# Performance work log

Measured on AMD Instinct MI355X. Metric: run time of the kernel, lower is better.

## Reference

```python
import jax, jax.numpy as jnp
import numpy as np

EPS = 1e-05
BITW = 8
BITA = 8


def _ste_round(v):
    # round with identity gradient (TF Round->Identity override)
    return v + jax.lax.stop_gradient(jnp.round(v) - v)


def _quantize_overflow(x, bits):
    # tensorlayer _quantize_overflow: linear quantization over [min, max]
    n = 2.0 ** bits - 1.0
    mx = jnp.max(x)
    mn = jnp.min(x)
    step = jax.lax.stop_gradient((mx - mn) / n)
    return _ste_round((x - mn) / step) * step + mn


def _conv2d_same(x, w):
    # x: [N,H,W,C], w: [KH,KW,C,F]
    return jax.lax.conv_general_dilated(
        x, w, window_strides=(1, 1), padding='SAME',
        dimension_numbers=('NHWC', 'HWIO', 'NHWC'))


def setup_inputs() -> dict:
    key = jax.random.key(0)
    k1, k2 = jax.random.split(key)
    x = jax.random.normal(k1, (32, 56, 56, 128), dtype=jnp.float32)
    W = jax.random.normal(k2, (3, 3, 128, 256), dtype=jnp.float32) * 0.02
    gamma = jnp.ones((256,), dtype=jnp.float32)
    beta = jnp.zeros((256,), dtype=jnp.float32)
    return {"x": x, "W": W, "gamma": gamma, "beta": beta}


def reference(x, W, gamma, beta):
    # 1) fake-quantize activations
    xq = _quantize_overflow(x, BITA)
    # 2) full-precision conv to get batch statistics (training path)
    conv_out = _conv2d_same(x, W)  # [N,H,W,F]
    mean = jnp.mean(conv_out, axis=(0, 1, 2))          # [F]
    var = jnp.var(conv_out, axis=(0, 1, 2))            # [F], biased (tf.nn.moments)
    inv_std = 1.0 / jnp.sqrt(var + EPS)                # [F]
    # 3) fold BN into weights/bias
    w_fold = W * (gamma * inv_std)                     # broadcast over [KH,KW,C,F]
    bias_fold = beta - gamma * mean * inv_std          # [F]
    # 4) quantize folded weights, conv with quantized activations
    wq = _quantize_overflow(w_fold, BITW)
    out = _conv2d_same(xq, wq) + bias_fold
    return jax.nn.relu(out)
```

## Files before the change

### kernel.cpp

```cpp
#include <hip/hip_runtime.h>

typedef float f32x4_t __attribute__((ext_vector_type(4)));
typedef __bf16 bf16x8_t __attribute__((ext_vector_type(8)));
typedef unsigned short u16x8_t __attribute__((ext_vector_type(8)));

#define NPIX        100352
#define PIX_PER_IMG 3136
#define PH          58
#define PPIX        3364
#define C_IN        128
#define C_OUT       256
#define NTAPS       9
#define NV4         3211264
#define NWELEM      294912
#define MTILES      392
#define NPADPIX     107648

#define OFF_ENC     0
#define OFF_SCALE   64
#define OFF_BIAS    1152
#define OFF_WT      4096
#define OFF_WQT     593920
#define OFF_PSUM    1183744
#define OFF_PSQ     1986560
#define OFF_XPAD    2789376
#define OFF_XQPAD   30347264

__device__ __forceinline__ unsigned short f2bf(float x) {
  unsigned u = __float_as_uint(x);
  u += 0x7FFFu + ((u >> 16) & 1u);
  return (unsigned short)(u >> 16);
}
__device__ __forceinline__ unsigned encf(float v) {
  unsigned u = __float_as_uint(v);
  return (u & 0x80000000u) ? ~u : (u | 0x80000000u);
}
__device__ __forceinline__ float decf(unsigned e) {
  unsigned u = (e & 0x80000000u) ? (e ^ 0x80000000u) : ~e;
  return __uint_as_float(u);
}
__device__ __forceinline__ void gl_lds16(const void* g, void* l) {
  auto gp = (const __attribute__((address_space(1))) unsigned*)(const unsigned*)g;
  auto lp = (__attribute__((address_space(3))) unsigned*)(unsigned*)l;
  __builtin_amdgcn_global_load_lds(gp, lp, 16, 0, 0);
}
#define SCHED_FENCE() __builtin_amdgcn_sched_barrier(0)

__global__ void kinit(unsigned* enc) {
  enc[0] = 0xFFFFFFFFu;
  enc[1] = 0u;
  enc[2] = 0xFFFFFFFFu;
  enc[3] = 0u;
}

__global__ void kminmax(const float4* __restrict__ x, unsigned* __restrict__ enc) {
  const int tid = blockIdx.x * blockDim.x + threadIdx.x;
  const int stride = gridDim.x * blockDim.x;
  float mn = 3.4e38f, mx = -3.4e38f;
  for (int i = tid; i < NV4; i += stride) {
    float4 v = x[i];
    mn = fminf(mn, fminf(fminf(v.x, v.y), fminf(v.z, v.w)));
    mx = fmaxf(mx, fmaxf(fmaxf(v.x, v.y), fmaxf(v.z, v.w)));
  }
  #pragma unroll
  for (int off = 32; off > 0; off >>= 1) {
    mn = fminf(mn, __shfl_xor(mn, off));
    mx = fmaxf(mx, __shfl_xor(mx, off));
  }
  __shared__ float smn[4], smx[4];
  const int lane = threadIdx.x & 63, w = threadIdx.x >> 6;
  if (lane == 0) { smn[w] = mn; smx[w] = mx; }
  __syncthreads();
  if (threadIdx.x == 0) {
    mn = fminf(fminf(smn[0], smn[1]), fminf(smn[2], smn[3]));
    mx = fmaxf(fmaxf(smx[0], smx[1]), fmaxf(smx[2], smx[3]));
    atomicMin(&enc[0], encf(mn));
    atomicMax(&enc[1], encf(mx));
  }
}

__global__ void kwconv(const float* __restrict__ W, unsigned short* __restrict__ wt) {
  const int idx = blockIdx.x * 256 + threadIdx.x;
  if (idx >= NWELEM) return;
  const int c = idx & 127;
  const int f = (idx >> 7) & 255;
  const int tap = idx >> 15;
  wt[idx] = f2bf(W[(tap * 128 + c) * 256 + f]);
}

__global__ void kwq(const float* __restrict__ W, const float* __restrict__ scale,
                    const unsigned* __restrict__ enc, unsigned short* __restrict__ wqt) {
  const int idx = blockIdx.x * 256 + threadIdx.x;
  if (idx >= NWELEM) return;
  const int c = idx & 127;
  const int f = (idx >> 7) & 255;
  const int tap = idx >> 15;
  const float wmn = decf(enc[2]), wmx = decf(enc[3]);
  const float wstep = (wmx - wmn) / 255.0f;
  const float wrstep = 255.0f / (wmx - wmn);
  const float v = W[(tap * 128 + c) * 256 + f] * scale[f];
  const float q = rintf((v - wmn) * wrstep) * wstep + wmn;
  wqt[idx] = f2bf(q);
}

__global__ void kpadfill(const float* __restrict__ x, const unsigned* __restrict__ enc,
                         unsigned short* __restrict__ xpad, unsigned short* __restrict__ xqpad)
{
  const int tid = blockIdx.x * 256 + threadIdx.x;
  if (tid >= NPADPIX * 16) return;
  const int pp = tid >> 4;
  const int c8 = (tid & 15) << 3;
  const int n = pp / PPIX;
  const int rem = pp - n * PPIX;
  const int hp = rem / PH;
  const int wp = rem - hp * PH;
  u16x8_t vb, vq;
  #pragma unroll
  for (int j = 0; j < 8; ++j) { vb[j] = 0; vq[j] = 0; }
  if (hp >= 1 && hp <= 56 && wp >= 1 && wp <= 56) {
    const float mn = decf(enc[0]), mx = decf(enc[1]);
    const float step = (mx - mn) / 255.0f, rstep = 255.0f / (mx - mn);
    const float* src = x + ((n * PIX_PER_IMG) + (hp - 1) * 56 + (wp - 1)) * C_IN + c8;
    const float4 a = *(const float4*)src;
    const float4 b = *(const float4*)(src + 4);
    const float v[8] = {a.x, a.y, a.z, a.w, b.x, b.y, b.z, b.w};
    #pragma unroll
    for (int j = 0; j < 8; ++j) {
      vb[j] = f2bf(v[j]);
      const float qv = rintf((v[j] - mn) * rstep) * step + mn;
      vq[j] = f2bf(qv);
    }
  }
  *(u16x8_t*)(xpad + pp * C_IN + c8) = vb;
  *(u16x8_t*)(xqpad + pp * C_IN + c8) = vq;
}

template<int STATS>
__global__ __launch_bounds__(512, 2)
void kconv(const unsigned short* __restrict__ xin,
           const unsigned short* __restrict__ wt,
           float* __restrict__ out,
           const float* __restrict__ bias,
           float* __restrict__ psum,
           float* __restrict__ psq)
{
  const int bid = blockIdx.x;
  const int bm = (bid & 7) * 49 + (bid >> 3);

  const int tid = threadIdx.x;
  const int lane = tid & 63;
  const int wid = tid >> 6;
  const int wm = wid >> 2;
  const int wn = wid & 3;
  const int l16 = lane & 15;
  const int rsub = lane >> 4;

  __shared__ __align__(16) unsigned char smem[131072];

  const int lchunk = (tid & 7) ^ ((tid >> 3) & 7);

  unsigned aoff[4];
  #pragma unroll
  for (int j = 0; j < 4; ++j) {
    const int pix = bm * 256 + j * 64 + (tid >> 3);
    const int n = pix / PIX_PER_IMG;
    const int rem = pix - n * PIX_PER_IMG;
    const int hh = rem / 56;
    const int ww = rem - hh * 56;
    aoff[j] = (unsigned)((n * PPIX + hh * PH + ww) * C_IN + lchunk * 8);
  }
  unsigned boff[4];
  #pragma unroll
  for (int j = 0; j < 4; ++j) {
    const int f = j * 64 + (tid >> 3);
    boff[j] = (unsigned)(f * C_IN + lchunk * 8);
  }

  f32x4_t acc[8][4];
  #pragma unroll
  for (int im = 0; im < 8; ++im)
    #pragma unroll
    for (int in = 0; in < 4; ++in)
      #pragma unroll
      for (int j = 0; j < 4; ++j) acc[im][in][j] = 0.f;

  auto stage = [&](int bsel, int s) {
    const int tap = s >> 1;
    const int chalf = (s & 1) << 6;
    const int kh = tap / 3, kw = tap - kh * 3;
    const unsigned atap = (unsigned)((kh * PH + kw) * C_IN + chalf);
    const unsigned btap = (unsigned)(tap * C_OUT * C_IN + chalf);
    unsigned char* sA = smem + bsel * 65536;
    unsigned char* sB = sA + 32768;
    #pragma unroll
    for (int j = 0; j < 4; ++j)
      gl_lds16(xin + atap + aoff[j], sA + j * 8192 + wid * 1024);
    #pragma unroll
    for (int j = 0; j < 4; ++j)
      gl_lds16(wt + btap + boff[j], sB + j * 8192 + wid * 1024);
  };

  auto compute = [&](int bsel) {
    const unsigned char* sA = smem + bsel * 65536;
    const unsigned char* sB = sA + 32768;
    #pragma unroll
    for (int ks = 0; ks < 2; ++ks) {
      const int c = ks * 4 + rsub;
      const int p = c ^ (l16 & 7);
      bf16x8_t av[8], bv[4];
      #pragma unroll
      for (int im = 0; im < 8; ++im)
        av[im] = *(const bf16x8_t*)(sA + (wm * 128 + im * 16 + l16) * 128 + p * 16);
      #pragma unroll
      for (int in = 0; in < 4; ++in)
        bv[in] = *(const bf16x8_t*)(sB + (wn * 64 + in * 16 + l16) * 128 + p * 16);
      #pragma unroll
      for (int im = 0; im < 8; ++im)
        #pragma unroll
        for (int in = 0; in < 4; ++in)
          acc[im][in] = __builtin_amdgcn_mfma_f32_16x16x32_bf16(av[im], bv[in], acc[im][in], 0, 0, 0);
    }
  };

  stage(0, 0);
  stage(1, 1);

  #pragma unroll 1
  for (int t = 0; t < 17; ++t) {
    asm volatile("s_waitcnt vmcnt(8)" ::: "memory");
    SCHED_FENCE();
    __builtin_amdgcn_s_barrier();
    SCHED_FENCE();
    compute(t & 1);
    SCHED_FENCE();
    __builtin_amdgcn_s_barrier();
    SCHED_FENCE();
    if (t < 16) stage(t & 1, t + 2);
  }
  asm volatile("s_waitcnt vmcnt(0)" ::: "memory");
  SCHED_FENCE();
  __builtin_amdgcn_s_barrier();
  SCHED_FENCE();
  compute(1);

  if (STATS) {
    float* sb = (float*)smem;
    #pragma unroll
    for (int in = 0; in < 4; ++in) {
      float s = 0.f, q = 0.f;
      #pragma unroll
      for (int im = 0; im < 8; ++im)
        #pragma unroll
        for (int j = 0; j < 4; ++j) {
          const float v = acc[im][in][j];
          s += v; q += v * v;
        }
      s += __shfl_xor(s, 16); q += __shfl_xor(q, 16);
      s += __shfl_xor(s, 32); q += __shfl_xor(q, 32);
      if (lane < 16) {
        sb[wid * 64 + in * 16 + lane] = s;
        sb[512 + wid * 64 + in * 16 + lane] = q;
      }
    }
    __syncthreads();
    if (tid < 256) {
      const int wn2 = tid >> 6, cl = tid & 63;
      const float s = sb[wn2 * 64 + cl] + sb[(4 + wn2) * 64 + cl];
      const float q = sb[512 + wn2 * 64 + cl] + sb[512 + (4 + wn2) * 64 + cl];
      psum[bm * 256 + tid] = s;
      psq[bm * 256 + tid] = q;
    }
  } else {
    float bval[4];
    #pragma unroll
    for (int in = 0; in < 4; ++in)
      bval[in] = bias[wn * 64 + in * 16 + l16];
    #pragma unroll
    for (int im = 0; im < 8; ++im) {
      #pragma unroll
      for (int j = 0; j < 4; ++j) {
        const int pix = bm * 256 + wm * 128 + im * 16 + rsub * 4 + j;
        #pragma unroll
        for (int in = 0; in < 4; ++in) {
          const int f = wn * 64 + in * 16 + l16;
          out[pix * 256 + f] = fmaxf(acc[im][in][j] + bval[in], 0.f);
        }
      }
    }
  }
}

__global__ __launch_bounds__(256)
void kstats(const float* __restrict__ psum, const float* __restrict__ psq,
            const float* __restrict__ gamma, const float* __restrict__ beta,
            float* __restrict__ scale, float* __restrict__ bias)
{
  const int ch = blockIdx.x;
  float s = 0.f, q = 0.f;
  for (int bm = threadIdx.x; bm < MTILES; bm += 256) {
    s += psum[bm * 256 + ch];
    q += psq[bm * 256 + ch];
  }
  #pragma unroll
  for (int off = 32; off > 0; off >>= 1) {
    s += __shfl_xor(s, off);
    q += __shfl_xor(q, off);
  }
  __shared__ float ss[4], sq2[4];
  const int lane = threadIdx.x & 63, w = threadIdx.x >> 6;
  if (lane == 0) { ss[w] = s; sq2[w] = q; }
  __syncthreads();
  if (threadIdx.x == 0) {
    s = ss[0] + ss[1] + ss[2] + ss[3];
    q = sq2[0] + sq2[1] + sq2[2] + sq2[3];
    const float inv = 1.0f / (float)NPIX;
    const float mean = s * inv;
    const float var = q * inv - mean * mean;
    const float istd = 1.0f / sqrtf(var + 1e-5f);
    const float g = gamma[ch];
    scale[ch] = g * istd;
    bias[ch] = beta[ch] - g * mean * istd;
  }
}

__global__ __launch_bounds__(256)
void kwmm(const float* __restrict__ W, const float* __restrict__ scale,
          unsigned* __restrict__ enc)
{
  const int idx = blockIdx.x * 256 + threadIdx.x;
  float v = 0.f;
  if (idx < NWELEM) v = W[idx] * scale[idx & 255];
  float mn = v, mx = v;
  #pragma unroll
  for (int off = 32; off > 0; off >>= 1) {
    mn = fminf(mn, __shfl_xor(mn, off));
    mx = fmaxf(mx, __shfl_xor(mx, off));
  }
  __shared__ float rmn[4], rmx[4];
  const int lane = threadIdx.x & 63, w = threadIdx.x >> 6;
  if (lane == 0) { rmn[w] = mn; rmx[w] = mx; }
  __syncthreads();
  if (threadIdx.x == 0) {
    mn = fminf(fminf(rmn[0], rmn[1]), fminf(rmn[2], rmn[3]));
    mx = fmaxf(fmaxf(rmx[0], rmx[1]), fmaxf(rmx[2], rmx[3]));
    atomicMin(&enc[2], encf(mn));
    atomicMax(&enc[3], encf(mx));
  }
}

extern "C" void kernel_launch(void* const* d_in, const int* in_sizes, int n_in,
                              void* d_out, int out_size, void* d_ws, size_t ws_size,
                              hipStream_t stream)
{
  const float* x     = (const float*)d_in[0];
  const float* W     = (const float*)d_in[1];
  const float* gamma = (const float*)d_in[2];
  const float* beta  = (const float*)d_in[3];
  float* out = (float*)d_out;
  char* ws = (char*)d_ws;

  unsigned* enc        = (unsigned*)(ws + OFF_ENC);
  float* scale         = (float*)(ws + OFF_SCALE);
  float* bias          = (float*)(ws + OFF_BIAS);
  unsigned short* Wt   = (unsigned short*)(ws + OFF_WT);
  unsigned short* Wqt  = (unsigned short*)(ws + OFF_WQT);
  float* psum          = (float*)(ws + OFF_PSUM);
  float* psq           = (float*)(ws + OFF_PSQ);
  unsigned short* xpad  = (unsigned short*)(ws + OFF_XPAD);
  unsigned short* xqpad = (unsigned short*)(ws + OFF_XQPAD);

  kinit<<<1, 64, 0, stream>>>(enc);
  kminmax<<<1024, 256, 0, stream>>>((const float4*)x, enc);
  kwconv<<<1152, 256, 0, stream>>>(W, Wt);
  kpadfill<<<6728, 256, 0, stream>>>(x, enc, xpad, xqpad);
  kconv<1><<<MTILES, 512, 0, stream>>>(xpad, Wt, nullptr, nullptr, psum, psq);
  kstats<<<256, 256, 0, stream>>>(psum, psq, gamma, beta, scale, bias);
  kwmm<<<1152, 256, 0, stream>>>(W, scale, enc);
  kwq<<<1152, 256, 0, stream>>>(W, scale, enc, Wqt);
  kconv<0><<<MTILES, 512, 0, stream>>>(xqpad, Wqt, out, bias, nullptr, nullptr);
}
```

Measured before the change: 230.4 us.

## Split conv tiles across output-channel halves and stream weights directly to registers

New measurement: 281.6 us. +22.2%, slower.

```diff
diff --git a/kernel.cpp b/kernel.cpp
--- a/kernel.cpp
+++ b/kernel.cpp
@@ -136,7 +136,7 @@
 }
 
 template<int STATS>
-__global__ __launch_bounds__(512, 2)
+__global__ __launch_bounds__(256, 2)
 void kconv(const unsigned short* __restrict__ xin,
            const unsigned short* __restrict__ wt,
            float* __restrict__ out,
@@ -145,36 +145,37 @@
            float* __restrict__ psq)
 {
   const int bid = blockIdx.x;
-  const int bm = (bid & 7) * 49 + (bid >> 3);
+  const int slot = (bid & 7) * 98 + (bid >> 3);
+  const int bm = slot >> 1;
+  const int bn = slot & 1;
 
   const int tid = threadIdx.x;
   const int lane = tid & 63;
   const int wid = tid >> 6;
-  const int wm = wid >> 2;
-  const int wn = wid & 3;
+  const int wm = wid >> 1;
+  const int wn = wid & 1;
   const int l16 = lane & 15;
   const int rsub = lane >> 4;
 
-  __shared__ __align__(16) unsigned char smem[131072];
-
-  const int lchunk = (tid & 7) ^ ((tid >> 3) & 7);
-
-  unsigned aoff[4];
-  #pragma unroll
-  for (int j = 0; j < 4; ++j) {
-    const int pix = bm * 256 + j * 64 + (tid >> 3);
+  __shared__ __align__(16) unsigned char smem[65536];
+
+  const int lchunk = (lane & 7) ^ ((lane >> 3) & 7);
+  unsigned aoff[8];
+  #pragma unroll
+  for (int j = 0; j < 8; ++j) {
+    const int pix = bm * 256 + j * 32 + wid * 8 + (lane >> 3);
     const int n = pix / PIX_PER_IMG;
     const int rem = pix - n * PIX_PER_IMG;
     const int hh = rem / 56;
     const int ww = rem - hh * 56;
     aoff[j] = (unsigned)((n * PPIX + hh * PH + ww) * C_IN + lchunk * 8);
   }
-  unsigned boff[4];
-  #pragma unroll
-  for (int j = 0; j < 4; ++j) {
-    const int f = j * 64 + (tid >> 3);
-    boff[j] = (unsigned)(f * C_IN + lchunk * 8);
-  }
+  unsigned boff[4][2];
+  #pragma unroll
+  for (int in = 0; in < 4; ++in)
+    #pragma unroll
+    for (int ks = 0; ks < 2; ++ks)
+      boff[in][ks] = (unsigned)((bn * 128 + wn * 64 + in * 16 + l16) * C_IN + (ks * 4 + rsub) * 8);
 
   f32x4_t acc[8][4];
   #pragma unroll
@@ -189,59 +190,65 @@
     const int chalf = (s & 1) << 6;
     const int kh = tap / 3, kw = tap - kh * 3;
     const unsigned atap = (unsigned)((kh * PH + kw) * C_IN + chalf);
-    const unsigned btap = (unsigned)(tap * C_OUT * C_IN + chalf);
-    unsigned char* sA = smem + bsel * 65536;
-    unsigned char* sB = sA + 32768;
-    #pragma unroll
-    for (int j = 0; j < 4; ++j)
-      gl_lds16(xin + atap + aoff[j], sA + j * 8192 + wid * 1024);
-    #pragma unroll
-    for (int j = 0; j < 4; ++j)
-      gl_lds16(wt + btap + boff[j], sB + j * 8192 + wid * 1024);
+    unsigned char* sA = smem + bsel * 32768;
+    #pragma unroll
+    for (int j = 0; j < 8; ++j)
+      gl_lds16(xin + atap + aoff[j], sA + j * 4096 + wid * 1024);
   };
 
-  auto compute = [&](int bsel) {
-    const unsigned char* sA = smem + bsel * 65536;
-    const unsigned char* sB = sA + 32768;
+  bf16x8_t bvc[4][2], bvn[4][2];
+  auto loadB = [&](int s, bf16x8_t (&bv)[4][2]) {
+    const int tap = s >> 1;
+    const int chalf = (s & 1) << 6;
+    const unsigned short* bbase = wt + tap * (C_OUT * C_IN) + chalf;
+    #pragma unroll
+    for (int in = 0; in < 4; ++in)
+      #pragma unroll
+      for (int ks = 0; ks < 2; ++ks)
+        bv[in][ks] = *(const bf16x8_t*)(bbase + boff[in][ks]);
+  };
+
+  auto compute = [&](int bsel, bf16x8_t (&bv)[4][2]) {
+    const unsigned char* sA = smem + bsel * 32768;
     #pragma unroll
     for (int ks = 0; ks < 2; ++ks) {
-      const int c = ks * 4 + rsub;
-      const int p = c ^ (l16 & 7);
-      bf16x8_t av[8], bv[4];
+      const int p = (ks * 4 + rsub) ^ (l16 & 7);
+      bf16x8_t av[8];
       #pragma unroll
       for (int im = 0; im < 8; ++im)
         av[im] = *(const bf16x8_t*)(sA + (wm * 128 + im * 16 + l16) * 128 + p * 16);
-      #pragma unroll
-      for (int in = 0; in < 4; ++in)
-        bv[in] = *(const bf16x8_t*)(sB + (wn * 64 + in * 16 + l16) * 128 + p * 16);
       #pragma unroll
       for (int im = 0; im < 8; ++im)
         #pragma unroll
         for (int in = 0; in < 4; ++in)
-          acc[im][in] = __builtin_amdgcn_mfma_f32_16x16x32_bf16(av[im], bv[in], acc[im][in], 0, 0, 0);
+          acc[im][in] = __builtin_amdgcn_mfma_f32_16x16x32_bf16(av[im], bv[in][ks], acc[im][in], 0, 0, 0);
     }
   };
 
   stage(0, 0);
+  loadB(0, bvc);
   stage(1, 1);
 
   #pragma unroll 1
-  for (int t = 0; t < 17; ++t) {
+  for (int t = 0; t < 18; ++t) {
     asm volatile("s_waitcnt vmcnt(8)" ::: "memory");
     SCHED_FENCE();
     __builtin_amdgcn_s_barrier();
     SCHED_FENCE();
-    compute(t & 1);
+    if (t < 17) loadB(t + 1, bvn);
+    compute(t & 1, bvc);
+    SCHED_FENCE();
+    asm volatile("s_waitcnt lgkmcnt(0)" ::: "memory");
     SCHED_FENCE();
     __builtin_amdgcn_s_barrier();
     SCHED_FENCE();
     if (t < 16) stage(t & 1, t + 2);
-  }
-  asm volatile("s_waitcnt vmcnt(0)" ::: "memory");
-  SCHED_FENCE();
-  __builtin_amdgcn_s_barrier();
-  SCHED_FENCE();
-  compute(1);
+    #pragma unroll
+    for (int in = 0; in < 4; ++in)
+      #pragma unroll
+      for (int ks = 0; ks < 2; ++ks)
+        bvc[in][ks] = bvn[in][ks];
+  }
 
   if (STATS) {
     float* sb = (float*)smem;
@@ -259,22 +266,22 @@
       s += __shfl_xor(s, 32); q += __shfl_xor(q, 32);
       if (lane < 16) {
         sb[wid * 64 + in * 16 + lane] = s;
-        sb[512 + wid * 64 + in * 16 + lane] = q;
+        sb[256 + wid * 64 + in * 16 + lane] = q;
       }
     }
     __syncthreads();
-    if (tid < 256) {
+    if (tid < 128) {
       const int wn2 = tid >> 6, cl = tid & 63;
-      const float s = sb[wn2 * 64 + cl] + sb[(4 + wn2) * 64 + cl];
-      const float q = sb[512 + wn2 * 64 + cl] + sb[512 + (4 + wn2) * 64 + cl];
-      psum[bm * 256 + tid] = s;
-      psq[bm * 256 + tid] = q;
+      const float s = sb[(wn2)*64 + cl] + sb[(2 + wn2) * 64 + cl];
+      const float q = sb[256 + (wn2)*64 + cl] + sb[256 + (2 + wn2) * 64 + cl];
+      psum[(bm * 2 + bn) * 128 + tid] = s;
+      psq[(bm * 2 + bn) * 128 + tid] = q;
     }
   } else {
     float bval[4];
     #pragma unroll
     for (int in = 0; in < 4; ++in)
-      bval[in] = bias[wn * 64 + in * 16 + l16];
+      bval[in] = bias[bn * 128 + wn * 64 + in * 16 + l16];
     #pragma unroll
     for (int im = 0; im < 8; ++im) {
       #pragma unroll
@@ -282,7 +289,7 @@
         const int pix = bm * 256 + wm * 128 + im * 16 + rsub * 4 + j;
         #pragma unroll
         for (int in = 0; in < 4; ++in) {
-          const int f = wn * 64 + in * 16 + l16;
+          const int f = bn * 128 + wn * 64 + in * 16 + l16;
           out[pix * 256 + f] = fmaxf(acc[im][in][j] + bval[in], 0.f);
         }
       }
@@ -296,10 +303,11 @@
             float* __restrict__ scale, float* __restrict__ bias)
 {
   const int ch = blockIdx.x;
+  const int bn = ch >> 7, col = ch & 127;
   float s = 0.f, q = 0.f;
   for (int bm = threadIdx.x; bm < MTILES; bm += 256) {
-    s += psum[bm * 256 + ch];
-    q += psq[bm * 256 + ch];
+    s += psum[(bm * 2 + bn) * 128 + col];
+    q += psq[(bm * 2 + bn) * 128 + col];
   }
   #pragma unroll
   for (int off = 32; off > 0; off >>= 1) {
@@ -373,9 +381,9 @@
   kminmax<<<1024, 256, 0, stream>>>((const float4*)x, enc);
   kwconv<<<1152, 256, 0, stream>>>(W, Wt);
   kpadfill<<<6728, 256, 0, stream>>>(x, enc, xpad, xqpad);
-  kconv<1><<<MTILES, 512, 0, stream>>>(xpad, Wt, nullptr, nullptr, psum, psq);
+  kconv<1><<<784, 256, 0, stream>>>(xpad, Wt, nullptr, nullptr, psum, psq);
   kstats<<<256, 256, 0, stream>>>(psum, psq, gamma, beta, scale, bias);
   kwmm<<<1152, 256, 0, stream>>>(W, scale, enc);
   kwq<<<1152, 256, 0, stream>>>(W, scale, enc, Wqt);
-  kconv<0><<<MTILES, 512, 0, stream>>>(xqpad, Wqt, out, bias, nullptr, nullptr);
-}
+  kconv<0><<<784, 256, 0, stream>>>(xqpad, Wqt, out, bias, nullptr, nullptr);
+}
```

## Interleave global-to-LDS loads with MFMA phases in a ping-pong pipeline

Applied to the files above, without the earlier changes.

Result: slower. 240.0 us (+4.2%).

```diff
diff --git a/kernel.cpp b/kernel.cpp
--- a/kernel.cpp
+++ b/kernel.cpp
@@ -158,23 +158,26 @@
   __shared__ __align__(16) unsigned char smem[131072];
 
   const int lchunk = (tid & 7) ^ ((tid >> 3) & 7);
-
-  unsigned aoff[4];
-  #pragma unroll
-  for (int j = 0; j < 4; ++j) {
-    const int pix = bm * 256 + j * 64 + (tid >> 3);
-    const int n = pix / PIX_PER_IMG;
-    const int rem = pix - n * PIX_PER_IMG;
-    const int hh = rem / 56;
-    const int ww = rem - hh * 56;
-    aoff[j] = (unsigned)((n * PPIX + hh * PH + ww) * C_IN + lchunk * 8);
-  }
-  unsigned boff[4];
-  #pragma unroll
-  for (int j = 0; j < 4; ++j) {
-    const int f = j * 64 + (tid >> 3);
-    boff[j] = (unsigned)(f * C_IN + lchunk * 8);
-  }
+  unsigned aoffA[2][2];
+  #pragma unroll
+  for (int h = 0; h < 2; ++h)
+    #pragma unroll
+    for (int j = 0; j < 2; ++j) {
+      const int pix = bm * 256 + h * 128 + j * 64 + (tid >> 3);
+      const int n = pix / PIX_PER_IMG;
+      const int rem = pix - n * PIX_PER_IMG;
+      const int hh = rem / 56;
+      const int ww = rem - hh * 56;
+      aoffA[h][j] = (unsigned)((n * PPIX + hh * PH + ww) * C_IN + lchunk * 8);
+    }
+  unsigned boffB[2][2];
+  #pragma unroll
+  for (int h = 0; h < 2; ++h)
+    #pragma unroll
+    for (int j = 0; j < 2; ++j) {
+      const int f = h * 128 + j * 64 + (tid >> 3);
+      boffB[h][j] = (unsigned)(f * C_IN + lchunk * 8);
+    }
 
   f32x4_t acc[8][4];
   #pragma unroll
@@ -184,64 +187,85 @@
       #pragma unroll
       for (int j = 0; j < 4; ++j) acc[im][in][j] = 0.f;
 
-  auto stage = [&](int bsel, int s) {
-    const int tap = s >> 1;
-    const int chalf = (s & 1) << 6;
-    const int kh = tap / 3, kw = tap - kh * 3;
-    const unsigned atap = (unsigned)((kh * PH + kw) * C_IN + chalf);
-    const unsigned btap = (unsigned)(tap * C_OUT * C_IN + chalf);
-    unsigned char* sA = smem + bsel * 65536;
-    unsigned char* sB = sA + 32768;
-    #pragma unroll
-    for (int j = 0; j < 4; ++j)
-      gl_lds16(xin + atap + aoff[j], sA + j * 8192 + wid * 1024);
-    #pragma unroll
-    for (int j = 0; j < 4; ++j)
-      gl_lds16(wt + btap + boff[j], sB + j * 8192 + wid * 1024);
-  };
-
-  auto compute = [&](int bsel) {
-    const unsigned char* sA = smem + bsel * 65536;
+  {
+    const unsigned atap0 = 0 * C_IN;
+    #pragma unroll
+    for (int h = 0; h < 2; ++h)
+      #pragma unroll
+      for (int j = 0; j < 2; ++j)
+        gl_lds16(xin + atap0 + aoffA[h][j], smem + h * 16384 + j * 8192 + wid * 1024);
+    #pragma unroll
+    for (int h = 0; h < 2; ++h)
+      #pragma unroll
+      for (int j = 0; j < 2; ++j)
+        gl_lds16(wt + boffB[h][j], smem + 32768 + h * 16384 + j * 8192 + wid * 1024);
+  }
+
+  #pragma unroll 1
+  for (int t = 0; t < 18; ++t) {
+    const int cb = t & 1;
+    const unsigned char* sA = smem + cb * 65536;
     const unsigned char* sB = sA + 32768;
-    #pragma unroll
-    for (int ks = 0; ks < 2; ++ks) {
-      const int c = ks * 4 + rsub;
-      const int p = c ^ (l16 & 7);
-      bf16x8_t av[8], bv[4];
-      #pragma unroll
-      for (int im = 0; im < 8; ++im)
-        av[im] = *(const bf16x8_t*)(sA + (wm * 128 + im * 16 + l16) * 128 + p * 16);
-      #pragma unroll
-      for (int in = 0; in < 4; ++in)
-        bv[in] = *(const bf16x8_t*)(sB + (wn * 64 + in * 16 + l16) * 128 + p * 16);
-      #pragma unroll
-      for (int im = 0; im < 8; ++im)
+    unsigned char* dA = smem + (cb ^ 1) * 65536;
+    unsigned char* dB = dA + 32768;
+    const int tn = t + 1;
+    const int tapn = tn >> 1;
+    const int khn = tapn / 3, kwn = tapn - khn * 3;
+    const unsigned atapn = (unsigned)((khn * PH + kwn) * C_IN + ((tn & 1) << 6));
+    const unsigned btapn = (unsigned)(tapn * (C_OUT * C_IN) + ((tn & 1) << 6));
+
+    #pragma unroll
+    for (int p = 0; p < 4; ++p) {
+      if (t < 17) {
+        if (p < 2) {
+          #pragma unroll
+          for (int j = 0; j < 2; ++j)
+            gl_lds16(xin + atapn + aoffA[p][j], dA + p * 16384 + j * 8192 + wid * 1024);
+        } else {
+          #pragma unroll
+          for (int j = 0; j < 2; ++j)
+            gl_lds16(wt + btapn + boffB[p - 2][j], dB + (p - 2) * 16384 + j * 8192 + wid * 1024);
+        }
+      }
+      if (p == 0) {
+        if (t < 17) asm volatile("s_waitcnt vmcnt(2)" ::: "memory");
+        else        asm volatile("s_waitcnt vmcnt(0)" ::: "memory");
+        SCHED_FENCE();
+        __builtin_amdgcn_s_barrier();
+        SCHED_FENCE();
+      }
+      const int h = p >> 1, ks = p & 1;
+      const int pc = (ks * 4 + rsub) ^ (l16 & 7);
+      bf16x8_t av[4], bv[4];
+      #pragma unroll
+      for (int i = 0; i < 4; ++i) {
+        const int rh = h * 64 + i * 16 + l16;
+        av[i] = *(const bf16x8_t*)(sA + wm * 16384 + rh * 128 + pc * 16);
+      }
+      #pragma unroll
+      for (int in = 0; in < 4; ++in) {
+        const int rb = (wn & 1) * 64 + in * 16 + l16;
+        bv[in] = *(const bf16x8_t*)(sB + (wn >> 1) * 16384 + rb * 128 + pc * 16);
+      }
+      if (p != 0) {
+        SCHED_FENCE();
+        __builtin_amdgcn_s_barrier();
+        SCHED_FENCE();
+      }
+      asm volatile("s_waitcnt lgkmcnt(0)" ::: "memory");
+      SCHED_FENCE();
+      __builtin_amdgcn_s_setprio(1);
+      #pragma unroll
+      for (int i = 0; i < 4; ++i)
         #pragma unroll
         for (int in = 0; in < 4; ++in)
-          acc[im][in] = __builtin_amdgcn_mfma_f32_16x16x32_bf16(av[im], bv[in], acc[im][in], 0, 0, 0);
-    }
-  };
-
-  stage(0, 0);
-  stage(1, 1);
-
-  #pragma unroll 1
-  for (int t = 0; t < 17; ++t) {
-    asm volatile("s_waitcnt vmcnt(8)" ::: "memory");
-    SCHED_FENCE();
-    __builtin_amdgcn_s_barrier();
-    SCHED_FENCE();
-    compute(t & 1);
-    SCHED_FENCE();
-    __builtin_amdgcn_s_barrier();
-    SCHED_FENCE();
-    if (t < 16) stage(t & 1, t + 2);
-  }
-  asm volatile("s_waitcnt vmcnt(0)" ::: "memory");
-  SCHED_FENCE();
-  __builtin_amdgcn_s_barrier();
-  SCHED_FENCE();
-  compute(1);
+          acc[h * 4 + i][in] = __builtin_amdgcn_mfma_f32_16x16x32_bf16(av[i], bv[in], acc[h * 4 + i][in], 0, 0, 0);
+      __builtin_amdgcn_s_setprio(0);
+      SCHED_FENCE();
+      __builtin_amdgcn_s_barrier();
+      SCHED_FENCE();
+    }
+  }
 
   if (STATS) {
     float* sb = (float*)smem;
```
